# Kernel optimization log

Hardware: AMD Instinct MI355X
Metric: run time of the kernel (lower is better)

Reference implementation:

```python
import jax, jax.numpy as jnp
import numpy as np

B, DIM, H, W = 512, 256, 14, 14
HEADS, KD, VD = 4, 16, 64  # key_dim=16, val_dim=attn_ratio*key_dim=64
RES = 14


def _bn(x, g, b, rm, rv, eps=1e-5):
    # eval-mode BatchNorm2d folded into per-channel affine
    s = g / jnp.sqrt(rv + eps)
    return x * s[None, :, None, None] + (b - rm * s)[None, :, None, None]


def setup_inputs() -> dict:
    key = jax.random.key(0)
    ks = jax.random.split(key, 6)
    # relative position bias index table: offset (|dy|,|dx|) -> flat index
    ii = np.arange(RES * RES)
    ry, rx = ii // RES, ii % RES
    dyo = np.abs(ry[:, None] - ry[None, :])
    dxo = np.abs(rx[:, None] - rx[None, :])
    bias_idxs = jnp.asarray(dyo * RES + dxo, dtype=jnp.int32)  # [196,196]
    QKV_OUT = 2 * KD + VD  # 96
    inp = {
        'x': jax.random.normal(ks[0], (B, DIM, H, W), jnp.float32),
        'qkv_w': jax.random.normal(ks[1], (HEADS, QKV_OUT, DIM // HEADS), jnp.float32) * 0.05,
        'qkv_g': jnp.ones((HEADS, QKV_OUT), jnp.float32),
        'qkv_b': jnp.zeros((HEADS, QKV_OUT), jnp.float32),
        'qkv_rm': jnp.zeros((HEADS, QKV_OUT), jnp.float32),
        'qkv_rv': jnp.ones((HEADS, QKV_OUT), jnp.float32),
        'dw_w': jax.random.normal(ks[2], (HEADS, KD, 1, 5, 5), jnp.float32) * 0.05,
        'dw_g': jnp.ones((HEADS, KD), jnp.float32),
        'dw_b': jnp.zeros((HEADS, KD), jnp.float32),
        'dw_rm': jnp.zeros((HEADS, KD), jnp.float32),
        'dw_rv': jnp.ones((HEADS, KD), jnp.float32),
        'proj_w': jax.random.normal(ks[3], (DIM, VD * HEADS), jnp.float32) * 0.05,
        'proj_g': jnp.ones((DIM,), jnp.float32),
        'proj_b': jnp.zeros((DIM,), jnp.float32),
        'proj_rm': jnp.zeros((DIM,), jnp.float32),
        'proj_rv': jnp.ones((DIM,), jnp.float32),
        'attn_biases': jax.random.normal(ks[4], (HEADS, RES * RES), jnp.float32) * 0.02,
        'bias_idxs': bias_idxs,
    }
    return inp


def reference(x, qkv_w, qkv_g, qkv_b, qkv_rm, qkv_rv,
              dw_w, dw_g, dw_b, dw_rm, dw_rv,
              proj_w, proj_g, proj_b, proj_rm, proj_rv,
              attn_biases, bias_idxs):
    Bc, C, Hc, Wc = x.shape
    N = Hc * Wc
    scale = KD ** -0.5
    bias = attn_biases[:, bias_idxs]  # [HEADS, N, N]
    chunks = jnp.split(x, HEADS, axis=1)  # per-head [B, dim//heads, H, W]
    feat = chunks[0]
    outs = []
    for h in range(HEADS):  # cascading residual -> inherently sequential over heads
        if h > 0:
            feat = feat + chunks[h]
        f = jnp.einsum('oc,bchw->bohw', qkv_w[h], feat)  # 1x1 conv
        f = _bn(f, qkv_g[h], qkv_b[h], qkv_rm[h], qkv_rv[h])
        q, k, v = f[:, :KD], f[:, KD:2 * KD], f[:, 2 * KD:]
        # 5x5 depthwise conv on q, padding 2
        q = jax.lax.conv_general_dilated(
            q, dw_w[h], window_strides=(1, 1), padding=[(2, 2), (2, 2)],
            dimension_numbers=('NCHW', 'OIHW', 'NCHW'), feature_group_count=KD)
        q = _bn(q, dw_g[h], dw_b[h], dw_rm[h], dw_rv[h])
        qf = q.reshape(Bc, KD, N) * scale
        kf = k.reshape(Bc, KD, N)
        vf = v.reshape(Bc, VD, N)
        attn = jnp.einsum('bdn,bdm->bnm', qf, kf) + bias[h]  # [B, N, N]
        attn = jax.nn.softmax(attn, axis=-1)
        feat = jnp.einsum('bdm,bnm->bdn', vf, attn).reshape(Bc, VD, Hc, Wc)
        outs.append(feat)
    y = jax.nn.relu(jnp.concatenate(outs, axis=1))  # [B, VD*HEADS, H, W]
    y = jnp.einsum('oc,bchw->bohw', proj_w, y)
    return _bn(y, proj_g, proj_b, proj_rm, proj_rv)
```

## Files before the change

kernel.cpp:

```cpp
#include <hip/hip_runtime.h>
#include <math.h>

#define BATCH 512
#define DIM 256
#define HEADS 4
#define KD 16
#define VD 64
#define NQ 196
#define CHW (DIM * NQ)

typedef __attribute__((ext_vector_type(8))) short short8;
typedef __attribute__((ext_vector_type(4))) float f32x4;

#define MFMA16(A, B, C) __builtin_amdgcn_mfma_f32_16x16x32_bf16((A), (B), (C), 0, 0, 0)

__device__ __forceinline__ unsigned short f2bf(float f) {
    unsigned int u = __float_as_uint(f);
    u += 0x7FFFu + ((u >> 16) & 1u);
    return (unsigned short)(u >> 16);
}
__device__ __forceinline__ float bf2f(unsigned short h) {
    return __uint_as_float(((unsigned int)h) << 16);
}
__device__ __forceinline__ void split8(const float* __restrict__ p, short8& hi, short8& lo) {
    float v[8];
    *(float4*)&v[0] = *(const float4*)p;
    *(float4*)&v[4] = *(const float4*)(p + 4);
    #pragma unroll
    for (int j = 0; j < 8; ++j) {
        unsigned short h = f2bf(v[j]);
        hi[j] = (short)h;
        lo[j] = (short)f2bf(v[j] - bf2f(h));
    }
}

#define OFF_QCH   0
#define OFF_QCL   16640
#define OFF_QRAW  33280
#define OFF_KBH   46592
#define OFF_KBL   64512
#define OFF_VBH   82432
#define OFF_VBL   112128
#define OFF_P     141824
#define OFF_DEN4  158464
#define OFF_SB    161792
#define OFF_TB    162176
#define OFF_DWS   162560
#define OFF_DWT   162624
#define SMEM_BYTES 162688

__global__ __launch_bounds__(256)
void bias_expand_kernel(const float* __restrict__ attn_biases,
                        const int* __restrict__ bias_idxs,
                        float* __restrict__ biasg) {
    int i = blockIdx.x * 256 + threadIdx.x;
    const int total = HEADS * NQ * NQ;
    if (i < total) {
        int h = i / (NQ * NQ);
        int r = i - h * (NQ * NQ);
        biasg[i] = attn_biases[h * NQ + bias_idxs[r]];
    }
}

__global__ __launch_bounds__(1024, 4)
void cascade_attn_kernel(const float* __restrict__ x,
                         const float* __restrict__ qkv_w,
                         const float* __restrict__ qkv_g,
                         const float* __restrict__ qkv_b,
                         const float* __restrict__ qkv_rm,
                         const float* __restrict__ qkv_rv,
                         const float* __restrict__ dw_w,
                         const float* __restrict__ dw_g,
                         const float* __restrict__ dw_b,
                         const float* __restrict__ dw_rm,
                         const float* __restrict__ dw_rv,
                         const float* __restrict__ biasg,
                         unsigned short* __restrict__ yrelu) {
    extern __shared__ __align__(16) char smem[];
    unsigned short* featU = (unsigned short*)(smem + OFF_QCH);
    unsigned short* qcH   = (unsigned short*)(smem + OFF_QCH);
    unsigned short* qcL   = (unsigned short*)(smem + OFF_QCL);
    float*          qraw  = (float*)(smem + OFF_QRAW);
    unsigned short* kbH   = (unsigned short*)(smem + OFF_KBH);
    unsigned short* kbL   = (unsigned short*)(smem + OFF_KBL);
    unsigned short* vbH   = (unsigned short*)(smem + OFF_VBH);
    unsigned short* vbL   = (unsigned short*)(smem + OFF_VBL);
    unsigned short* Pb    = (unsigned short*)(smem + OFF_P);
    float*          den4  = (float*)(smem + OFF_DEN4);
    float*          sbT   = (float*)(smem + OFF_SB);
    float*          tbT   = (float*)(smem + OFF_TB);
    float*          dwsT  = (float*)(smem + OFF_DWS);
    float*          dwtT  = (float*)(smem + OFF_DWT);

    const int b    = blockIdx.x;
    const int tid  = threadIdx.x;
    const int w    = tid >> 6;
    const int li   = tid & 15;
    const int quad = (tid >> 4) & 3;

    for (int t = tid; t < SMEM_BYTES / 4; t += 1024) ((unsigned int*)smem)[t] = 0u;
    __syncthreads();
    for (int t = tid; t < VD * NQ; t += 1024) {
        int n = t % NQ, c = t / NQ;
        featU[n * 72 + c] = f2bf(x[((size_t)b * DIM + c) * NQ + n]);
    }
    __syncthreads();

    for (int h = 0; h < HEADS; ++h) {
        if (tid < 96) {
            float s = qkv_g[h * 96 + tid] * rsqrtf(qkv_rv[h * 96 + tid] + 1e-5f);
            sbT[tid] = s;
            tbT[tid] = qkv_b[h * 96 + tid] - qkv_rm[h * 96 + tid] * s;
        } else if (tid < 112) {
            int c = tid - 96;
            float s = dw_g[h * 16 + c] * rsqrtf(dw_rv[h * 16 + c] + 1e-5f);
            dwsT[c] = s;
            dwtT[c] = dw_b[h * 16 + c] - dw_rm[h * 16 + c] * s;
        }
        __syncthreads();

        for (int T = w; T < 78; T += 16) {
            int ot = T / 13, nt = T - ot * 13;
            const float* wrow = qkv_w + ((size_t)h * 96 + ot * 16 + li) * 64;
            short8 ah0, al0, ah1, al1;
            split8(wrow + quad * 8, ah0, al0);
            split8(wrow + 32 + quad * 8, ah1, al1);
            short8 b0 = *(const short8*)(featU + (nt * 16 + li) * 72 + quad * 8);
            short8 b1 = *(const short8*)(featU + (nt * 16 + li) * 72 + 32 + quad * 8);
            f32x4 acc = {0.f, 0.f, 0.f, 0.f};
            acc = MFMA16(ah0, b0, acc);
            acc = MFMA16(al0, b0, acc);
            acc = MFMA16(ah1, b1, acc);
            acc = MFMA16(al1, b1, acc);
            int n = nt * 16 + li;
            bool nok = (n < NQ);
            #pragma unroll
            for (int r = 0; r < 4; ++r) {
                int o = ot * 16 + quad * 4 + r;
                float val = acc[r] * sbT[o] + tbT[o];
                if (nok) {
                    if (o < 16) {
                        qraw[o * 208 + n] = val;
                    } else if (o < 32) {
                        int c = o - 16;
                        unsigned short hh = f2bf(val);
                        kbH[n * 40 + c] = hh;
                        kbL[n * 40 + c] = f2bf(val - bf2f(hh));
                    } else {
                        int d = o - 32;
                        unsigned short hh = f2bf(val);
                        vbH[d * 232 + n] = hh;
                        vbL[d * 232 + n] = f2bf(val - bf2f(hh));
                    }
                }
            }
        }
        __syncthreads();

        for (int t = tid; t < KD * NQ; t += 1024) {
            int n = t % NQ, c = t / NQ;
            int py = n / 14, px = n - py * 14;
            const float* qr = qraw + c * 208;
            const float* wdc = dw_w + ((size_t)h * KD + c) * 25;
            float accv = 0.f;
            #pragma unroll
            for (int ky = 0; ky < 5; ++ky) {
                int yy = py + ky - 2;
                if (yy < 0 || yy >= 14) continue;
                #pragma unroll
                for (int kx = 0; kx < 5; ++kx) {
                    int xx = px + kx - 2;
                    if (xx < 0 || xx >= 14) continue;
                    accv = fmaf(wdc[ky * 5 + kx], qr[yy * 14 + xx], accv);
                }
            }
            float val = fmaf(accv, dwsT[c], dwtT[c]) * 0.25f;
            unsigned short hh = f2bf(val);
            qcH[n * 40 + c] = hh;
            qcL[n * 40 + c] = f2bf(val - bf2f(hh));
            qcH[n * 40 + 16 + c] = 0;
            qcL[n * 40 + 16 + c] = 0;
        }
        if (tid < 832) den4[tid] = 0.f;
        __syncthreads();

        f32x4 pacc[4];
        #pragma unroll
        for (int s = 0; s < 4; ++s) pacc[s] = (f32x4){0.f, 0.f, 0.f, 0.f};

        for (int mi = 0; mi < 7; ++mi) {
            for (int T = w; T < 26; T += 16) {
                int s = (T >= 13) ? 1 : 0;
                int nt = T - s * 13;
                int n0 = nt * 16;
                int mg = mi * 32 + s * 16 + li;
                float bias4[4];
                #pragma unroll
                for (int r = 0; r < 4; ++r) {
                    int n = n0 + quad * 4 + r;
                    int ni = n < NQ ? n : NQ - 1;
                    int mgi = mg < NQ ? mg : NQ - 1;
                    bias4[r] = biasg[(size_t)h * (NQ * NQ) + ni * NQ + mgi];
                }
                short8 qh = *(const short8*)(qcH + (n0 + li) * 40 + quad * 8);
                short8 ql = *(const short8*)(qcL + (n0 + li) * 40 + quad * 8);
                short8 kh = *(const short8*)(kbH + mg * 40 + quad * 8);
                short8 kl = *(const short8*)(kbL + mg * 40 + quad * 8);
                f32x4 acc = {0.f, 0.f, 0.f, 0.f};
                acc = MFMA16(qh, kh, acc);
                acc = MFMA16(qh, kl, acc);
                acc = MFMA16(ql, kh, acc);
                bool mok = (mg < NQ);
                #pragma unroll
                for (int r = 0; r < 4; ++r) {
                    float e = mok ? __expf(acc[r] + bias4[r]) : 0.f;
                    int n = n0 + quad * 4 + r;
                    Pb[n * 40 + s * 16 + li] = f2bf(e);
                }
            }
            __syncthreads();

            if (tid < 832) {
                int n = tid >> 2, part = tid & 3;
                short8 pv = *(const short8*)(Pb + n * 40 + part * 8);
                float sum = 0.f;
                #pragma unroll
                for (int j = 0; j < 8; ++j) sum += bf2f((unsigned short)pv[j]);
                den4[n * 4 + part] += sum;
            }
            {
                int slot = 0;
                for (int T = w; T < 52; T += 16, ++slot) {
                    int dt = T / 13, nt = T - dt * 13;
                    short8 p  = *(const short8*)(Pb + (nt * 16 + li) * 40 + quad * 8);
                    short8 vh = *(const short8*)(vbH + (dt * 16 + li) * 232 + mi * 32 + quad * 8);
                    short8 vl = *(const short8*)(vbL + (dt * 16 + li) * 232 + mi * 32 + quad * 8);
                    pacc[slot] = MFMA16(p, vh, pacc[slot]);
                    pacc[slot] = MFMA16(p, vl, pacc[slot]);
                }
            }
            __syncthreads();
        }

        {
            int slot = 0;
            for (int T = w; T < 52; T += 16, ++slot) {
                int dt = T / 13, nt = T - dt * 13;
                int d = dt * 16 + li;
                #pragma unroll
                for (int r = 0; r < 4; ++r) {
                    int n = nt * 16 + quad * 4 + r;
                    if (n < NQ) {
                        f32x4 dv = *(const f32x4*)(den4 + n * 4);
                        float dn = (dv.x + dv.y) + (dv.z + dv.w);
                        float val = pacc[slot][r] / dn;
                        featU[n * 72 + d] = f2bf(val);
                    }
                }
            }
        }
        __syncthreads();

        for (int t = tid; t < (VD * NQ) / 8; t += 1024) {
            int n  = t >> 3;
            int c0 = (t & 7) * 8;
            short8 u = *(const short8*)(featU + n * 72 + c0);
            short8 ru;
            #pragma unroll
            for (int j = 0; j < 8; ++j) {
                unsigned short uu = (unsigned short)u[j];
                ru[j] = (short)((uu & 0x8000u) ? (unsigned short)0 : uu);
            }
            *(short8*)(yrelu + ((size_t)b * NQ + n) * DIM + h * VD + c0) = ru;
        }
        __syncthreads();

        if (h < 3) {
            for (int t = tid; t < VD * NQ; t += 1024) {
                int n = t % NQ, c = t / NQ;
                float v = bf2f(featU[n * 72 + c]) + x[((size_t)b * DIM + (h + 1) * VD + c) * NQ + n];
                featU[n * 72 + c] = f2bf(v);
            }
            for (int t = tid; t < 12 * 64; t += 1024)
                featU[(NQ + t / 64) * 72 + (t & 63)] = 0;
        }
        __syncthreads();
    }
}

__global__ __launch_bounds__(512, 4)
void proj_kernel(const unsigned short* __restrict__ X,
                 const float* __restrict__ W,
                 const float* __restrict__ pg,
                 const float* __restrict__ pb,
                 const float* __restrict__ prm,
                 const float* __restrict__ prv,
                 float* __restrict__ out) {
    __shared__ __align__(16) unsigned short Xs[2][128 * 40];
    const int tid  = threadIdx.x;
    const int w    = tid >> 6;
    const int li   = tid & 15;
    const int quad = (tid >> 4) & 3;
    const int jb   = blockIdx.x * 128;

    const int jl = tid >> 2;
    const int c0 = (tid & 3) * 8;
    const unsigned short* xsrc = X + (size_t)(jb + jl) * 256 + c0;

    f32x4 acc[2][8];
    #pragma unroll
    for (int ot = 0; ot < 2; ++ot)
        #pragma unroll
        for (int jt = 0; jt < 8; ++jt) acc[ot][jt] = (f32x4){0.f, 0.f, 0.f, 0.f};

    *(short8*)(&Xs[0][jl * 40 + c0]) = *(const short8*)(xsrc);
    __syncthreads();

    const float* wr0 = W + (size_t)(w * 32 + li) * 256 + quad * 8;
    const float* wr1 = wr0 + 16 * 256;

    for (int ks = 0; ks < 8; ++ks) {
        const int cur = ks & 1;
        short8 nv;
        if (ks < 7) nv = *(const short8*)(xsrc + (ks + 1) * 32);
        short8 ah0, al0, ah1, al1;
        split8(wr0 + ks * 32, ah0, al0);
        split8(wr1 + ks * 32, ah1, al1);
        #pragma unroll
        for (int jt = 0; jt < 8; ++jt) {
            short8 bx = *(const short8*)(&Xs[cur][(jt * 16 + li) * 40 + quad * 8]);
            acc[0][jt] = MFMA16(ah0, bx, acc[0][jt]);
            acc[0][jt] = MFMA16(al0, bx, acc[0][jt]);
            acc[1][jt] = MFMA16(ah1, bx, acc[1][jt]);
            acc[1][jt] = MFMA16(al1, bx, acc[1][jt]);
        }
        if (ks < 7) {
            *(short8*)(&Xs[cur ^ 1][jl * 40 + c0]) = nv;
            __syncthreads();
        }
    }

    #pragma unroll
    for (int ot = 0; ot < 2; ++ot) {
        #pragma unroll
        for (int r = 0; r < 4; ++r) {
            int o = w * 32 + ot * 16 + quad * 4 + r;
            float s = pg[o] * rsqrtf(prv[o] + 1e-5f);
            float t = pb[o] - prm[o] * s;
            #pragma unroll
            for (int jt = 0; jt < 8; ++jt) {
                int j = jb + jt * 16 + li;
                int bb = j / NQ;
                int n = j - bb * NQ;
                out[(size_t)bb * CHW + (size_t)o * NQ + n] = fmaf(acc[ot][jt][r], s, t);
            }
        }
    }
}

extern "C" void kernel_launch(void* const* d_in, const int* in_sizes, int n_in,
                              void* d_out, int out_size, void* d_ws, size_t ws_size,
                              hipStream_t stream) {
    const float* x        = (const float*)d_in[0];
    const float* qkv_w    = (const float*)d_in[1];
    const float* qkv_g    = (const float*)d_in[2];
    const float* qkv_b    = (const float*)d_in[3];
    const float* qkv_rm   = (const float*)d_in[4];
    const float* qkv_rv   = (const float*)d_in[5];
    const float* dw_w     = (const float*)d_in[6];
    const float* dw_g     = (const float*)d_in[7];
    const float* dw_b     = (const float*)d_in[8];
    const float* dw_rm    = (const float*)d_in[9];
    const float* dw_rv    = (const float*)d_in[10];
    const float* proj_w   = (const float*)d_in[11];
    const float* proj_g   = (const float*)d_in[12];
    const float* proj_b   = (const float*)d_in[13];
    const float* proj_rm  = (const float*)d_in[14];
    const float* proj_rv  = (const float*)d_in[15];
    const float* attn_bs  = (const float*)d_in[16];
    const int*   bias_idx = (const int*)d_in[17];

    float* biasg = (float*)d_ws;
    unsigned short* yrelu = (unsigned short*)((char*)d_ws + 614656);

    {
        int total = HEADS * NQ * NQ;
        hipLaunchKernelGGL(bias_expand_kernel, dim3((total + 255) / 256), dim3(256),
                           0, stream, attn_bs, bias_idx, biasg);
    }
    hipLaunchKernelGGL(cascade_attn_kernel, dim3(BATCH), dim3(1024),
                       SMEM_BYTES, stream,
                       x, qkv_w, qkv_g, qkv_b, qkv_rm, qkv_rv,
                       dw_w, dw_g, dw_b, dw_rm, dw_rv, biasg, yrelu);
    hipLaunchKernelGGL(proj_kernel, dim3(784), dim3(512), 0, stream,
                       yrelu, proj_w, proj_g, proj_b, proj_rm, proj_rv,
                       (float*)d_out);
}
```

Before: 597.8 us.

## Pre-split weights, merge QK MFMAs, double-buffer P and prefetch next-head input

The bf16 hi/lo split of qkv_w and proj_w moves into a one-time prep kernel, so the attention and projection kernels load pre-split shorts instead of converting floats on every tile. The QK^T product packs q hi/lo into one K=32 operand against duplicated k tiles, which needs two MFMAs instead of three. The probability tile is double-buffered so the next score/exp pass overlaps the PV accumulation of the current one, removing one barrier per step. Next-head x values are prefetched into registers, index math is made incremental, and bias reads become float4 loads using the transposed (symmetric) bias layout. The cost is more registers and LDS traffic, plus reliance on the bias table being symmetric.

```diff
diff --git a/kernel.cpp b/kernel.cpp
--- a/kernel.cpp
+++ b/kernel.cpp
@@ -22,26 +22,15 @@
 __device__ __forceinline__ float bf2f(unsigned short h) {
     return __uint_as_float(((unsigned int)h) << 16);
 }
-__device__ __forceinline__ void split8(const float* __restrict__ p, short8& hi, short8& lo) {
-    float v[8];
-    *(float4*)&v[0] = *(const float4*)p;
-    *(float4*)&v[4] = *(const float4*)(p + 4);
-    #pragma unroll
-    for (int j = 0; j < 8; ++j) {
-        unsigned short h = f2bf(v[j]);
-        hi[j] = (short)h;
-        lo[j] = (short)f2bf(v[j] - bf2f(h));
-    }
-}
-
-#define OFF_QCH   0
-#define OFF_QCL   16640
-#define OFF_QRAW  33280
-#define OFF_KBH   46592
-#define OFF_KBL   64512
-#define OFF_VBH   82432
-#define OFF_VBL   112128
-#define OFF_P     141824
+
+#define OFF_QC    0
+#define OFF_P0    16640
+#define OFF_P1    33280
+#define OFF_QRAW  49920
+#define OFF_KB1   63232
+#define OFF_KB2   81152
+#define OFF_VBH   99072
+#define OFF_VBL   128768
 #define OFF_DEN4  158464
 #define OFF_SB    161792
 #define OFF_TB    162176
@@ -50,21 +39,42 @@
 #define SMEM_BYTES 162688
 
 __global__ __launch_bounds__(256)
-void bias_expand_kernel(const float* __restrict__ attn_biases,
-                        const int* __restrict__ bias_idxs,
-                        float* __restrict__ biasg) {
+void prep_kernel(const float* __restrict__ attn_biases,
+                 const int* __restrict__ bias_idxs,
+                 const float* __restrict__ qkv_w,
+                 const float* __restrict__ proj_w,
+                 float* __restrict__ biasg,
+                 unsigned short* __restrict__ whH,
+                 unsigned short* __restrict__ whL,
+                 unsigned short* __restrict__ pwH,
+                 unsigned short* __restrict__ pwL) {
     int i = blockIdx.x * 256 + threadIdx.x;
-    const int total = HEADS * NQ * NQ;
-    if (i < total) {
+    const int T1 = HEADS * NQ * NQ;
+    const int T2 = HEADS * 96 * 64;
+    const int T3 = DIM * DIM;
+    if (i < T1) {
         int h = i / (NQ * NQ);
         int r = i - h * (NQ * NQ);
         biasg[i] = attn_biases[h * NQ + bias_idxs[r]];
+    } else if (i < T1 + T2) {
+        int j = i - T1;
+        float v = qkv_w[j];
+        unsigned short hh = f2bf(v);
+        whH[j] = hh;
+        whL[j] = f2bf(v - bf2f(hh));
+    } else if (i < T1 + T2 + T3) {
+        int j = i - T1 - T2;
+        float v = proj_w[j];
+        unsigned short hh = f2bf(v);
+        pwH[j] = hh;
+        pwL[j] = f2bf(v - bf2f(hh));
     }
 }
 
 __global__ __launch_bounds__(1024, 4)
 void cascade_attn_kernel(const float* __restrict__ x,
-                         const float* __restrict__ qkv_w,
+                         const unsigned short* __restrict__ whH,
+                         const unsigned short* __restrict__ whL,
                          const float* __restrict__ qkv_g,
                          const float* __restrict__ qkv_b,
                          const float* __restrict__ qkv_rm,
@@ -77,15 +87,15 @@
                          const float* __restrict__ biasg,
                          unsigned short* __restrict__ yrelu) {
     extern __shared__ __align__(16) char smem[];
-    unsigned short* featU = (unsigned short*)(smem + OFF_QCH);
-    unsigned short* qcH   = (unsigned short*)(smem + OFF_QCH);
-    unsigned short* qcL   = (unsigned short*)(smem + OFF_QCL);
+    unsigned short* featU = (unsigned short*)(smem + OFF_QC);
+    unsigned short* qc    = (unsigned short*)(smem + OFF_QC);
+    unsigned short* Pb0   = (unsigned short*)(smem + OFF_P0);
+    unsigned short* Pb1   = (unsigned short*)(smem + OFF_P1);
     float*          qraw  = (float*)(smem + OFF_QRAW);
-    unsigned short* kbH   = (unsigned short*)(smem + OFF_KBH);
-    unsigned short* kbL   = (unsigned short*)(smem + OFF_KBL);
+    unsigned short* kb1   = (unsigned short*)(smem + OFF_KB1);
+    unsigned short* kb2   = (unsigned short*)(smem + OFF_KB2);
     unsigned short* vbH   = (unsigned short*)(smem + OFF_VBH);
     unsigned short* vbL   = (unsigned short*)(smem + OFF_VBL);
-    unsigned short* Pb    = (unsigned short*)(smem + OFF_P);
     float*          den4  = (float*)(smem + OFF_DEN4);
     float*          sbT   = (float*)(smem + OFF_SB);
     float*          tbT   = (float*)(smem + OFF_TB);
@@ -97,16 +107,33 @@
     const int w    = tid >> 6;
     const int li   = tid & 15;
     const int quad = (tid >> 4) & 3;
+    const int tn0  = tid % NQ;
+    const int tc0  = tid / NQ;
 
     for (int t = tid; t < SMEM_BYTES / 4; t += 1024) ((unsigned int*)smem)[t] = 0u;
     __syncthreads();
-    for (int t = tid; t < VD * NQ; t += 1024) {
-        int n = t % NQ, c = t / NQ;
-        featU[n * 72 + c] = f2bf(x[((size_t)b * DIM + c) * NQ + n]);
+    {
+        int n = tn0, c = tc0;
+        #pragma unroll
+        for (int i = 0; i < 13; ++i) {
+            int t = tid + i * 1024;
+            if (t < VD * NQ) featU[n * 72 + c] = f2bf(x[((size_t)b * DIM + c) * NQ + n]);
+            n += 44; c += 5; if (n >= NQ) { n -= NQ; ++c; }
+        }
     }
     __syncthreads();
 
     for (int h = 0; h < HEADS; ++h) {
+        float xpre[13];
+        if (h < 3) {
+            int n = tn0, c = tc0;
+            #pragma unroll
+            for (int i = 0; i < 13; ++i) {
+                int t = tid + i * 1024;
+                if (t < VD * NQ) xpre[i] = x[((size_t)b * DIM + (h + 1) * VD + c) * NQ + n];
+                n += 44; c += 5; if (n >= NQ) { n -= NQ; ++c; }
+            }
+        }
         if (tid < 96) {
             float s = qkv_g[h * 96 + tid] * rsqrtf(qkv_rv[h * 96 + tid] + 1e-5f);
             sbT[tid] = s;
@@ -121,10 +148,11 @@
 
         for (int T = w; T < 78; T += 16) {
             int ot = T / 13, nt = T - ot * 13;
-            const float* wrow = qkv_w + ((size_t)h * 96 + ot * 16 + li) * 64;
-            short8 ah0, al0, ah1, al1;
-            split8(wrow + quad * 8, ah0, al0);
-            split8(wrow + 32 + quad * 8, ah1, al1);
+            const size_t wb = ((size_t)h * 96 + ot * 16 + li) * 64;
+            short8 ah0 = *(const short8*)(whH + wb + quad * 8);
+            short8 al0 = *(const short8*)(whL + wb + quad * 8);
+            short8 ah1 = *(const short8*)(whH + wb + 32 + quad * 8);
+            short8 al1 = *(const short8*)(whL + wb + 32 + quad * 8);
             short8 b0 = *(const short8*)(featU + (nt * 16 + li) * 72 + quad * 8);
             short8 b1 = *(const short8*)(featU + (nt * 16 + li) * 72 + 32 + quad * 8);
             f32x4 acc = {0.f, 0.f, 0.f, 0.f};
@@ -144,8 +172,9 @@
                     } else if (o < 32) {
                         int c = o - 16;
                         unsigned short hh = f2bf(val);
-                        kbH[n * 40 + c] = hh;
-                        kbL[n * 40 + c] = f2bf(val - bf2f(hh));
+                        kb1[n * 40 + c] = hh;
+                        kb1[n * 40 + 16 + c] = hh;
+                        kb2[n * 40 + c] = f2bf(val - bf2f(hh));
                     } else {
                         int d = o - 32;
                         unsigned short hh = f2bf(val);
@@ -157,29 +186,31 @@
         }
         __syncthreads();
 
-        for (int t = tid; t < KD * NQ; t += 1024) {
-            int n = t % NQ, c = t / NQ;
-            int py = n / 14, px = n - py * 14;
-            const float* qr = qraw + c * 208;
-            const float* wdc = dw_w + ((size_t)h * KD + c) * 25;
-            float accv = 0.f;
-            #pragma unroll
-            for (int ky = 0; ky < 5; ++ky) {
-                int yy = py + ky - 2;
-                if (yy < 0 || yy >= 14) continue;
+        {
+            int n = tn0, c = tc0, py = tn0 / 14, px = tn0 - (tn0 / 14) * 14;
+            for (int t = tid; t < KD * NQ; t += 1024) {
+                const float* qr = qraw + c * 208;
+                const float* wdc = dw_w + ((size_t)h * KD + c) * 25;
+                float accv = 0.f;
                 #pragma unroll
-                for (int kx = 0; kx < 5; ++kx) {
-                    int xx = px + kx - 2;
-                    if (xx < 0 || xx >= 14) continue;
-                    accv = fmaf(wdc[ky * 5 + kx], qr[yy * 14 + xx], accv);
-                }
-            }
-            float val = fmaf(accv, dwsT[c], dwtT[c]) * 0.25f;
-            unsigned short hh = f2bf(val);
-            qcH[n * 40 + c] = hh;
-            qcL[n * 40 + c] = f2bf(val - bf2f(hh));
-            qcH[n * 40 + 16 + c] = 0;
-            qcL[n * 40 + 16 + c] = 0;
+                for (int ky = 0; ky < 5; ++ky) {
+                    int yy = py + ky - 2;
+                    if (yy < 0 || yy >= 14) continue;
+                    #pragma unroll
+                    for (int kx = 0; kx < 5; ++kx) {
+                        int xx = px + kx - 2;
+                        if (xx < 0 || xx >= 14) continue;
+                        accv = fmaf(wdc[ky * 5 + kx], qr[yy * 14 + xx], accv);
+                    }
+                }
+                float val = fmaf(accv, dwsT[c], dwtT[c]) * 0.25f;
+                unsigned short hh = f2bf(val);
+                qc[n * 40 + c] = hh;
+                qc[n * 40 + 16 + c] = f2bf(val - bf2f(hh));
+                n += 44; c += 5; px += 2; py += 3;
+                if (px >= 14) { px -= 14; ++py; }
+                if (n >= NQ) { n -= NQ; ++c; py -= 14; }
+            }
         }
         if (tid < 832) den4[tid] = 0.f;
         __syncthreads();
@@ -188,41 +219,53 @@
         #pragma unroll
         for (int s = 0; s < 4; ++s) pacc[s] = (f32x4){0.f, 0.f, 0.f, 0.f};
 
-        for (int mi = 0; mi < 7; ++mi) {
+        auto spass = [&](int mi2, unsigned short* __restrict__ PbW) {
             for (int T = w; T < 26; T += 16) {
                 int s = (T >= 13) ? 1 : 0;
                 int nt = T - s * 13;
                 int n0 = nt * 16;
-                int mg = mi * 32 + s * 16 + li;
-                float bias4[4];
-                #pragma unroll
-                for (int r = 0; r < 4; ++r) {
-                    int n = n0 + quad * 4 + r;
-                    int ni = n < NQ ? n : NQ - 1;
-                    int mgi = mg < NQ ? mg : NQ - 1;
-                    bias4[r] = biasg[(size_t)h * (NQ * NQ) + ni * NQ + mgi];
-                }
-                short8 qh = *(const short8*)(qcH + (n0 + li) * 40 + quad * 8);
-                short8 ql = *(const short8*)(qcL + (n0 + li) * 40 + quad * 8);
-                short8 kh = *(const short8*)(kbH + mg * 40 + quad * 8);
-                short8 kl = *(const short8*)(kbL + mg * 40 + quad * 8);
+                int mg = mi2 * 32 + s * 16 + li;
+                bool mok = (mg < NQ);
+                float bias4[4] = {0.f, 0.f, 0.f, 0.f};
+                if (mok) {
+                    const float* bp = biasg + (size_t)h * (NQ * NQ) + mg * NQ;
+                    int nb = n0 + quad * 4;
+                    if (nb + 3 < NQ) {
+                        float4 bv = *(const float4*)(bp + nb);
+                        bias4[0] = bv.x; bias4[1] = bv.y; bias4[2] = bv.z; bias4[3] = bv.w;
+                    } else {
+                        #pragma unroll
+                        for (int r = 0; r < 4; ++r) {
+                            int ni = nb + r; if (ni > NQ - 1) ni = NQ - 1;
+                            bias4[r] = bp[ni];
+                        }
+                    }
+                }
+                short8 q  = *(const short8*)(qc  + (n0 + li) * 40 + quad * 8);
+                short8 k1 = *(const short8*)(kb1 + mg * 40 + quad * 8);
+                short8 k2 = *(const short8*)(kb2 + mg * 40 + quad * 8);
                 f32x4 acc = {0.f, 0.f, 0.f, 0.f};
-                acc = MFMA16(qh, kh, acc);
-                acc = MFMA16(qh, kl, acc);
-                acc = MFMA16(ql, kh, acc);
-                bool mok = (mg < NQ);
+                acc = MFMA16(q, k1, acc);
+                acc = MFMA16(q, k2, acc);
                 #pragma unroll
                 for (int r = 0; r < 4; ++r) {
                     float e = mok ? __expf(acc[r] + bias4[r]) : 0.f;
-                    int n = n0 + quad * 4 + r;
-                    Pb[n * 40 + s * 16 + li] = f2bf(e);
-                }
-            }
-            __syncthreads();
+                    PbW[(n0 + quad * 4 + r) * 40 + s * 16 + li] = f2bf(e);
+                }
+            }
+        };
+
+        spass(0, Pb0);
+        __syncthreads();
+
+        for (int mi = 0; mi < 7; ++mi) {
+            unsigned short* PbR = (mi & 1) ? Pb1 : Pb0;
+            unsigned short* PbW = (mi & 1) ? Pb0 : Pb1;
+            if (mi < 6) spass(mi + 1, PbW);
 
             if (tid < 832) {
                 int n = tid >> 2, part = tid & 3;
-                short8 pv = *(const short8*)(Pb + n * 40 + part * 8);
+                short8 pv = *(const short8*)(PbR + n * 40 + part * 8);
                 float sum = 0.f;
                 #pragma unroll
                 for (int j = 0; j < 8; ++j) sum += bf2f((unsigned short)pv[j]);
@@ -232,7 +275,7 @@
                 int slot = 0;
                 for (int T = w; T < 52; T += 16, ++slot) {
                     int dt = T / 13, nt = T - dt * 13;
-                    short8 p  = *(const short8*)(Pb + (nt * 16 + li) * 40 + quad * 8);
+                    short8 p  = *(const short8*)(PbR + (nt * 16 + li) * 40 + quad * 8);
                     short8 vh = *(const short8*)(vbH + (dt * 16 + li) * 232 + mi * 32 + quad * 8);
                     short8 vl = *(const short8*)(vbL + (dt * 16 + li) * 232 + mi * 32 + quad * 8);
                     pacc[slot] = MFMA16(p, vh, pacc[slot]);
@@ -276,10 +319,15 @@
         __syncthreads();
 
         if (h < 3) {
-            for (int t = tid; t < VD * NQ; t += 1024) {
-                int n = t % NQ, c = t / NQ;
-                float v = bf2f(featU[n * 72 + c]) + x[((size_t)b * DIM + (h + 1) * VD + c) * NQ + n];
-                featU[n * 72 + c] = f2bf(v);
+            int n = tn0, c = tc0;
+            #pragma unroll
+            for (int i = 0; i < 13; ++i) {
+                int t = tid + i * 1024;
+                if (t < VD * NQ) {
+                    float v = bf2f(featU[n * 72 + c]) + xpre[i];
+                    featU[n * 72 + c] = f2bf(v);
+                }
+                n += 44; c += 5; if (n >= NQ) { n -= NQ; ++c; }
             }
             for (int t = tid; t < 12 * 64; t += 1024)
                 featU[(NQ + t / 64) * 72 + (t & 63)] = 0;
@@ -290,7 +338,8 @@
 
 __global__ __launch_bounds__(512, 4)
 void proj_kernel(const unsigned short* __restrict__ X,
-                 const float* __restrict__ W,
+                 const unsigned short* __restrict__ pwH,
+                 const unsigned short* __restrict__ pwL,
                  const float* __restrict__ pg,
                  const float* __restrict__ pb,
                  const float* __restrict__ prm,
@@ -316,16 +365,17 @@
     *(short8*)(&Xs[0][jl * 40 + c0]) = *(const short8*)(xsrc);
     __syncthreads();
 
-    const float* wr0 = W + (size_t)(w * 32 + li) * 256 + quad * 8;
-    const float* wr1 = wr0 + 16 * 256;
+    const unsigned short* pH = pwH + (size_t)(w * 32 + li) * 256 + quad * 8;
+    const unsigned short* pL = pwL + (size_t)(w * 32 + li) * 256 + quad * 8;
 
     for (int ks = 0; ks < 8; ++ks) {
         const int cur = ks & 1;
         short8 nv;
         if (ks < 7) nv = *(const short8*)(xsrc + (ks + 1) * 32);
-        short8 ah0, al0, ah1, al1;
-        split8(wr0 + ks * 32, ah0, al0);
-        split8(wr1 + ks * 32, ah1, al1);
+        short8 ah0 = *(const short8*)(pH + ks * 32);
+        short8 al0 = *(const short8*)(pL + ks * 32);
+        short8 ah1 = *(const short8*)(pH + 16 * 256 + ks * 32);
+        short8 al1 = *(const short8*)(pL + 16 * 256 + ks * 32);
         #pragma unroll
         for (int jt = 0; jt < 8; ++jt) {
             short8 bx = *(const short8*)(&Xs[cur][(jt * 16 + li) * 40 + quad * 8]);
@@ -380,19 +430,25 @@
     const float* attn_bs  = (const float*)d_in[16];
     const int*   bias_idx = (const int*)d_in[17];
 
-    float* biasg = (float*)d_ws;
-    unsigned short* yrelu = (unsigned short*)((char*)d_ws + 614656);
+    char* ws = (char*)d_ws;
+    float* biasg = (float*)ws;
+    unsigned short* yrelu = (unsigned short*)(ws + 614656);
+    unsigned short* whH = (unsigned short*)(ws + 51994880);
+    unsigned short* whL = (unsigned short*)(ws + 52044032);
+    unsigned short* pwH = (unsigned short*)(ws + 52093184);
+    unsigned short* pwL = (unsigned short*)(ws + 52224256);
 
     {
-        int total = HEADS * NQ * NQ;
-        hipLaunchKernelGGL(bias_expand_kernel, dim3((total + 255) / 256), dim3(256),
-                           0, stream, attn_bs, bias_idx, biasg);
+        int total = HEADS * NQ * NQ + HEADS * 96 * 64 + DIM * DIM;
+        hipLaunchKernelGGL(prep_kernel, dim3((total + 255) / 256), dim3(256),
+                           0, stream, attn_bs, bias_idx, qkv_w, proj_w,
+                           biasg, whH, whL, pwH, pwL);
     }
     hipLaunchKernelGGL(cascade_attn_kernel, dim3(BATCH), dim3(1024),
                        SMEM_BYTES, stream,
-                       x, qkv_w, qkv_g, qkv_b, qkv_rm, qkv_rv,
+                       x, whH, whL, qkv_g, qkv_b, qkv_rm, qkv_rv,
                        dw_w, dw_g, dw_b, dw_rm, dw_rv, biasg, yrelu);
     hipLaunchKernelGGL(proj_kernel, dim3(784), dim3(512), 0, stream,
-                       yrelu, proj_w, proj_g, proj_b, proj_rm, proj_rv,
+                       yrelu, pwH, pwL, proj_g, proj_b, proj_rm, proj_rv,
                        (float*)d_out);
 }
```

Result: slower. 615.8 us (+3.0%).
